# Kernel tuning notes

Measured on AMD Instinct MI355X. Metric: run time of the kernel, lower is better.

Reference implementation:

```python
import jax, jax.numpy as jnp
import numpy as np

NUM_HEADS = 12
EMB = 768
HEAD = 64
SEQ = 2048
BATCH = 2


def setup_inputs() -> dict:
    key = jax.random.key(0)
    ks = jax.random.split(key, 6)
    scale = 0.02
    x = jax.random.normal(ks[0], (BATCH, SEQ, EMB), dtype=jnp.float32)
    # per-head Q/K/V projections (bias-free, Karpathy-style HeadAttention), batched over heads
    Wq = jax.random.normal(ks[1], (NUM_HEADS, EMB, HEAD), dtype=jnp.float32) * scale
    Wk = jax.random.normal(ks[2], (NUM_HEADS, EMB, HEAD), dtype=jnp.float32) * scale
    Wv = jax.random.normal(ks[3], (NUM_HEADS, EMB, HEAD), dtype=jnp.float32) * scale
    # output projection: Linear(head_size*num_heads, emb_size)
    Wo = jax.random.normal(ks[4], (NUM_HEADS * HEAD, EMB), dtype=jnp.float32) * scale
    bo = jax.random.normal(ks[5], (EMB,), dtype=jnp.float32) * scale
    return {"x": x, "Wq": Wq, "Wk": Wk, "Wv": Wv, "Wo": Wo, "bo": bo}


def reference(x, Wq, Wk, Wv, Wo, bo):
    B, S, E = x.shape
    # batched per-head projections: [B,S,E] x [H,E,D] -> [B,H,S,D]
    q = jnp.einsum("bse,hed->bhsd", x, Wq)
    k = jnp.einsum("bse,hed->bhsd", x, Wk)
    v = jnp.einsum("bse,hed->bhsd", x, Wv)
    scale = 1.0 / jnp.sqrt(jnp.asarray(HEAD, dtype=x.dtype))
    scores = jnp.einsum("bhsd,bhtd->bhst", q, k) * scale  # [B,H,S,S]
    causal = jnp.tril(jnp.ones((S, S), dtype=bool))
    scores = jnp.where(causal, scores, jnp.asarray(-jnp.inf, dtype=scores.dtype))
    attn = jax.nn.softmax(scores, axis=-1)
    out = jnp.einsum("bhst,bhtd->bhsd", attn, v)  # [B,H,S,D]
    # concat heads along last dim: [B,S,H*D]
    out = out.transpose(0, 2, 1, 3).reshape(B, S, NUM_HEADS * HEAD)
    # output projection (dropout is identity in eval mode)
    return out @ Wo + bo
```

## Files before the change

kernel.cpp:

```cpp
#include <hip/hip_runtime.h>
#include <hip/hip_bf16.h>
#include <string.h>

#define NHEAD 12
#define EMB 768
#define HDD 64
#define SEQ 2048

typedef __attribute__((ext_vector_type(4))) float f32x4;
typedef __attribute__((ext_vector_type(8))) short short8;
typedef __attribute__((ext_vector_type(4))) short short4v;
typedef __attribute__((ext_vector_type(2))) unsigned uint2v;
typedef unsigned int u32;

#define GLL16(g, l)                                                            \
    __builtin_amdgcn_global_load_lds(                                          \
        (const __attribute__((address_space(1))) u32*)(g),                     \
        (__attribute__((address_space(3))) u32*)(l), 16, 0, 0)

static __device__ __forceinline__ short bf16s(float f) {
    unsigned u = __builtin_bit_cast(unsigned, f);
    u = (u + 0x7fffu + ((u >> 16) & 1u)) >> 16;
    return (short)u;
}
static __device__ __forceinline__ float bf2f(short s) {
    unsigned u = ((unsigned)(unsigned short)s) << 16;
    return __builtin_bit_cast(float, u);
}
static __device__ __forceinline__ float ex2(float x) {
    float r;
    asm("v_exp_f32 %0, %1" : "=v"(r) : "v"(x));
    return r;
}
static __device__ __forceinline__ unsigned pk2(float a, float b) {
    float2 f2;
    f2.x = a;
    f2.y = b;
    __hip_bfloat162 h = __float22bfloat162_rn(f2);
    unsigned r;
    memcpy(&r, &h, 4);
    return r;
}

__global__ void k_cvt_all(const float* __restrict__ x, const float* __restrict__ Wq,
                          const float* __restrict__ Wk, const float* __restrict__ Wv,
                          const float* __restrict__ Wo, short* __restrict__ xb,
                          short* __restrict__ WqT, short* __restrict__ WkT,
                          short* __restrict__ WvT, short* __restrict__ WoT) {
    const int bid = blockIdx.x, t = threadIdx.x;
    if (bid < 1536) {
        const int i = (bid * 256 + t) * 8;
        const f32x4* s = (const f32x4*)(x + i);
        f32x4 a = s[0], b = s[1];
        short8 o;
        o[0] = bf16s(a[0]); o[1] = bf16s(a[1]); o[2] = bf16s(a[2]); o[3] = bf16s(a[3]);
        o[4] = bf16s(b[0]); o[5] = bf16s(b[1]); o[6] = bf16s(b[2]); o[7] = bf16s(b[3]);
        *(short8*)(xb + i) = o;
    } else if (bid < 1968) {
        const int idx = bid - 1536;
        const int h = idx % 12, e0 = ((idx / 12) % 12) * 64, z = idx / 144;
        const float* W = z == 0 ? Wq : (z == 1 ? Wk : Wv);
        short* Wt = z == 0 ? WqT : (z == 1 ? WkT : WvT);
        __shared__ float tile[64][65];
        const int r = t >> 2, c0 = (t & 3) * 16;
        const float* src = W + (h * EMB + e0 + r) * HDD + c0;
#pragma unroll
        for (int i = 0; i < 16; ++i) tile[r][c0 + i] = src[i];
        __syncthreads();
        short* dst = Wt + (h * HDD + r) * EMB + e0 + c0;
#pragma unroll
        for (int i = 0; i < 16; ++i) dst[i] = bf16s(tile[c0 + i][r]);
    } else {
        const int idx = bid - 1968;
        const int k0 = (idx % 12) * 64, n0 = (idx / 12) * 64;
        __shared__ float tile[64][65];
        const int r = t >> 2, c0 = (t & 3) * 16;
        const float* src = Wo + (k0 + r) * EMB + n0 + c0;
#pragma unroll
        for (int i = 0; i < 16; ++i) tile[r][c0 + i] = src[i];
        __syncthreads();
        short* dst = WoT + (n0 + r) * EMB + k0 + c0;
#pragma unroll
        for (int i = 0; i < 16; ++i) dst[i] = bf16s(tile[c0 + i][r]);
    }
}

template <int MODE>
__global__ __launch_bounds__(256) void k_gemm(
        const short* __restrict__ xb, const short* __restrict__ Wt0,
        const short* __restrict__ Wt1, const short* __restrict__ Wt2,
        short* __restrict__ Qo, short* __restrict__ Ko, short* __restrict__ Vo,
        const float* __restrict__ bias, float* __restrict__ Fout) {
    __shared__ alignas(16) short As[2][128 * 32];
    __shared__ alignas(16) short Bs[2][128 * 32];
    const int t = threadIdx.x, lane = t & 63, wave = t >> 6;
    const int z = (MODE == 0) ? blockIdx.z : 0;
    const short* Ap;
    const short* Bp;
    int m0, n0;
    if (MODE == 1) {
        Ap = xb; Bp = Wt0; m0 = blockIdx.y * 128; n0 = blockIdx.x * 128;
    } else if (z == 0) {
        Ap = xb; Bp = Wt0; m0 = blockIdx.y * 128; n0 = blockIdx.x * 128;
    } else if (z == 1) {
        Ap = xb; Bp = Wt1; m0 = blockIdx.y * 128; n0 = blockIdx.x * 128;
    } else {
        Ap = Wt2; Bp = xb; m0 = blockIdx.x * 128; n0 = blockIdx.y * 128;
    }

    const int srow = lane >> 2;
    const int scolSw = ((lane & 3) ^ ((srow >> 1) & 3)) * 8;
    const short* gA = Ap + (long)(m0 + wave * 32 + srow) * EMB + scolSw;
    const short* gB = Bp + (long)(n0 + wave * 32 + srow) * EMB + scolSw;
    const int ldoff = (wave * 32) * 32;

    const int wm = (wave >> 1) * 64, wn = (wave & 1) * 64;
    const int fr = lane & 15, hi = lane >> 4;
    const int rdoff = (hi ^ ((fr >> 1) & 3)) * 8;

    f32x4 acc[4][4];
#pragma unroll
    for (int i = 0; i < 4; ++i)
#pragma unroll
        for (int j = 0; j < 4; ++j)
#pragma unroll
            for (int e = 0; e < 4; ++e) acc[i][j][e] = 0.f;

    GLL16(gA, &As[0][ldoff]);
    GLL16(gA + 16 * EMB, &As[0][ldoff + 16 * 32]);
    GLL16(gB, &Bs[0][ldoff]);
    GLL16(gB + 16 * EMB, &Bs[0][ldoff + 16 * 32]);
    __syncthreads();

    int cur = 0;
    for (int kk = 0; kk < EMB; kk += 32) {
        const int nxt = cur ^ 1;
        if (kk + 32 < EMB) {
            GLL16(gA + kk + 32, &As[nxt][ldoff]);
            GLL16(gA + kk + 32 + 16 * EMB, &As[nxt][ldoff + 16 * 32]);
            GLL16(gB + kk + 32, &Bs[nxt][ldoff]);
            GLL16(gB + kk + 32 + 16 * EMB, &Bs[nxt][ldoff + 16 * 32]);
        }
        const short* curA = &As[cur][0];
        const short* curB = &Bs[cur][0];
        short8 af[4], bfq[4];
#pragma unroll
        for (int i = 0; i < 4; ++i)
            af[i] = *(const short8*)(curA + (wm + i * 16 + fr) * 32 + rdoff);
#pragma unroll
        for (int j = 0; j < 4; ++j)
            bfq[j] = *(const short8*)(curB + (wn + j * 16 + fr) * 32 + rdoff);
#pragma unroll
        for (int i = 0; i < 4; ++i)
#pragma unroll
            for (int j = 0; j < 4; ++j)
                acc[i][j] = __builtin_amdgcn_mfma_f32_16x16x32_bf16(af[i], bfq[j], acc[i][j], 0, 0, 0);
        __syncthreads();
        cur = nxt;
    }

    const int r0 = hi * 4;
#pragma unroll
    for (int i = 0; i < 4; ++i) {
#pragma unroll
        for (int j = 0; j < 4; ++j) {
            const int nbase = n0 + wn + j * 16 + fr;
            float bj = 0.f;
            if (MODE == 1) bj = bias[nbase];
#pragma unroll
            for (int r = 0; r < 4; ++r) {
                const int m = m0 + wm + i * 16 + r0 + r;
                float v = acc[i][j][r];
                if (MODE == 0) {
                    if (z == 2) {
                        const int hh = m >> 6, dd = m & 63;
                        const int bb = nbase >> 11, ss = nbase & 2047;
                        Vo[(long)((bb * NHEAD + hh) * HDD + dd) * SEQ + ss] = bf16s(v);
                    } else {
                        const int bb = m >> 11, ss = m & 2047;
                        const int hh = nbase >> 6, dd = nbase & 63;
                        short* Dst = (z == 0) ? Qo : Ko;
                        if (z == 0) v *= 0.18033688f;
                        Dst[(long)((bb * NHEAD + hh) * SEQ + ss) * HDD + dd] = bf16s(v);
                    }
                } else {
                    Fout[(long)m * EMB + nbase] = v + bj;
                }
            }
        }
    }
}

__global__ __launch_bounds__(256) void k_attn(
        const short* __restrict__ Q, const short* __restrict__ K,
        const short* __restrict__ VT, short* __restrict__ O,
        short* __restrict__ Ub, float* __restrict__ Mb, float* __restrict__ Lb) {
    __shared__ alignas(16) short Kbuf[2][64 * 72];
    __shared__ alignas(16) short Vbuf[2][64 * 72];
    __shared__ alignas(16) short Ps[4][16 * 72];
    const int bh = blockIdx.x;
    const int h = bh % NHEAD, b = bh / NHEAD;
    const int yy = blockIdx.y;
    int qs, kb, ke, chunk, split;
    if (yy < 16)      { qs = 16 + yy; kb = 0;  ke = 16;     chunk = 0; split = 1; }
    else if (yy < 32) { qs = yy;      kb = 16; ke = qs + 1; chunk = 1; split = 1; }
    else              { qs = 47 - yy; kb = 0;  ke = qs + 1; chunk = 0; split = 0; }
    const int q0 = qs * 64;
    const int t = threadIdx.x, lane = t & 63, wave = t >> 6;
    const long base = (long)(b * NHEAD + h) * SEQ * HDD;
    const short* Qg = Q + base;
    const short* Kg = K + base;
    const short* Vg = VT + base;
    const int fr = lane & 15, hi = lane >> 4, fk = hi * 8, r0 = hi * 4;
    const int wq = q0 + wave * 16;

    short8 qf[2];
#pragma unroll
    for (int c = 0; c < 2; ++c)
        qf[c] = *(const short8*)(Qg + (long)(wq + fr) * HDD + c * 32 + fk);

    f32x4 oacc[4];
#pragma unroll
    for (int i = 0; i < 4; ++i)
#pragma unroll
        for (int e = 0; e < 4; ++e) oacc[i][e] = 0.f;
    float mrun = -3e38f, lrun = 0.f;

    const int srow = t >> 2, sc = (t & 3) * 16;
    const short* KgS = Kg + (long)srow * HDD + sc;
    const short* VgS = Vg + (long)srow * SEQ + sc;
    short* Pw = &Ps[wave][0];

    short8 kv0 = *(const short8*)(KgS + (long)(kb * 64) * HDD);
    short8 kv1 = *(const short8*)(KgS + (long)(kb * 64) * HDD + 8);
    short8 vv0 = *(const short8*)(VgS + kb * 64);
    short8 vv1 = *(const short8*)(VgS + kb * 64 + 8);
    *(short8*)(&Kbuf[0][srow * 72 + sc]) = kv0;
    *(short8*)(&Kbuf[0][srow * 72 + sc + 8]) = kv1;
    *(short8*)(&Vbuf[0][srow * 72 + sc]) = vv0;
    *(short8*)(&Vbuf[0][srow * 72 + sc + 8]) = vv1;
    if (ke - kb > 1) {
        kv0 = *(const short8*)(KgS + (long)(kb * 64 + 64) * HDD);
        kv1 = *(const short8*)(KgS + (long)(kb * 64 + 64) * HDD + 8);
        vv0 = *(const short8*)(VgS + kb * 64 + 64);
        vv1 = *(const short8*)(VgS + kb * 64 + 64 + 8);
    }
    __syncthreads();

    for (int kt = kb; kt < ke; ++kt) {
        const int k0 = kt * 64;
        const int cur = (kt - kb) & 1;
        if (kt + 1 < ke) {
            *(short8*)(&Kbuf[cur ^ 1][srow * 72 + sc]) = kv0;
            *(short8*)(&Kbuf[cur ^ 1][srow * 72 + sc + 8]) = kv1;
            *(short8*)(&Vbuf[cur ^ 1][srow * 72 + sc]) = vv0;
            *(short8*)(&Vbuf[cur ^ 1][srow * 72 + sc + 8]) = vv1;
            if (kt + 2 < ke) {
                kv0 = *(const short8*)(KgS + (long)(k0 + 128) * HDD);
                kv1 = *(const short8*)(KgS + (long)(k0 + 128) * HDD + 8);
                vv0 = *(const short8*)(VgS + (k0 + 128));
                vv1 = *(const short8*)(VgS + (k0 + 128) + 8);
            }
        }
        if (k0 <= wq + 15) {
            const short* Ks = &Kbuf[cur][0];
            const short* Vs = &Vbuf[cur][0];

            f32x4 st[4];
#pragma unroll
            for (int nt = 0; nt < 4; ++nt) {
                const short8 kf0 = *(const short8*)(Ks + (nt * 16 + fr) * 72 + fk);
                const short8 kf1 = *(const short8*)(Ks + (nt * 16 + fr) * 72 + 32 + fk);
#pragma unroll
                for (int e = 0; e < 4; ++e) st[nt][e] = 0.f;
                st[nt] = __builtin_amdgcn_mfma_f32_16x16x32_bf16(kf0, qf[0], st[nt], 0, 0, 0);
                st[nt] = __builtin_amdgcn_mfma_f32_16x16x32_bf16(kf1, qf[1], st[nt], 0, 0, 0);
            }

            float p[4][4];
            float pmax = -3e38f;
            if (k0 + 63 > wq) {
                const int myq = wq + fr;
#pragma unroll
                for (int nt = 0; nt < 4; ++nt)
#pragma unroll
                    for (int r = 0; r < 4; ++r) {
                        float s = st[nt][r];
                        if (k0 + nt * 16 + r0 + r > myq) s = -3e38f;
                        p[nt][r] = s;
                        pmax = fmaxf(pmax, s);
                    }
            } else {
#pragma unroll
                for (int nt = 0; nt < 4; ++nt)
#pragma unroll
                    for (int r = 0; r < 4; ++r) {
                        p[nt][r] = st[nt][r];
                        pmax = fmaxf(pmax, st[nt][r]);
                    }
            }
            pmax = fmaxf(pmax, __shfl_xor(pmax, 16, 64));
            pmax = fmaxf(pmax, __shfl_xor(pmax, 32, 64));
            const float mnew = fmaxf(mrun, pmax);
            const float corr = ex2(mrun - mnew);
            mrun = mnew;
            float rsum = 0.f;
#pragma unroll
            for (int nt = 0; nt < 4; ++nt)
#pragma unroll
                for (int r = 0; r < 4; ++r) {
                    const float e = ex2(p[nt][r] - mnew);
                    p[nt][r] = e;
                    rsum += e;
                }
            rsum += __shfl_xor(rsum, 16, 64);
            rsum += __shfl_xor(rsum, 32, 64);
            lrun = lrun * corr + rsum;
#pragma unroll
            for (int dt = 0; dt < 4; ++dt)
#pragma unroll
                for (int e = 0; e < 4; ++e) oacc[dt][e] *= corr;

#pragma unroll
            for (int nt = 0; nt < 4; ++nt) {
                uint2v w;
                w[0] = pk2(p[nt][0], p[nt][1]);
                w[1] = pk2(p[nt][2], p[nt][3]);
                *(uint2v*)(Pw + fr * 72 + nt * 16 + r0) = w;
            }

#pragma unroll
            for (int kc = 0; kc < 2; ++kc) {
                const short8 pf = *(const short8*)(Pw + fr * 72 + kc * 32 + fk);
#pragma unroll
                for (int dt = 0; dt < 4; ++dt) {
                    const short8 vf = *(const short8*)(Vs + (dt * 16 + fr) * 72 + kc * 32 + fk);
                    oacc[dt] = __builtin_amdgcn_mfma_f32_16x16x32_bf16(vf, pf, oacc[dt], 0, 0, 0);
                }
            }
        }
        __syncthreads();
    }

    if (split) {
        const int pidx = (bh * 16 + (qs - 16)) * 2 + chunk;
        short* Up = Ub + pidx * 4096;
#pragma unroll
        for (int dt = 0; dt < 4; ++dt)
#pragma unroll
            for (int r = 0; r < 4; ++r)
                Up[(dt * 16 + r0 + r) * 64 + wave * 16 + fr] = bf16s(oacc[dt][r]);
        if (lane < 16) {
            Mb[pidx * 64 + wave * 16 + lane] = mrun;
            Lb[pidx * 64 + wave * 16 + lane] = lrun;
        }
        return;
    }

    short* Os = &Ps[0][0];
    const float iv = 1.0f / lrun;
#pragma unroll
    for (int dt = 0; dt < 4; ++dt) {
        uint2v w;
        w[0] = pk2(oacc[dt][0] * iv, oacc[dt][1] * iv);
        w[1] = pk2(oacc[dt][2] * iv, oacc[dt][3] * iv);
        *(uint2v*)(Os + (wave * 16 + fr) * 72 + dt * 16 + r0) = w;
    }
    __syncthreads();
    {
        const int row = t >> 2, c0 = (t & 3) * 16;
        const short8 o0 = *(const short8*)(Os + row * 72 + c0);
        const short8 o1 = *(const short8*)(Os + row * 72 + c0 + 8);
        short* Og = O + (long)(b * SEQ + q0 + row) * EMB + h * HDD + c0;
        *(short8*)Og = o0;
        *(short8*)(Og + 8) = o1;
    }
}

__global__ __launch_bounds__(256) void k_merge(
        const short* __restrict__ Ub, const float* __restrict__ Mb,
        const float* __restrict__ Lb, short* __restrict__ O) {
    __shared__ float aS[64], bS[64], iL[64];
    __shared__ short tile[64 * 72];
    const int bid = blockIdx.x;
    const int bh = bid >> 4, sidx = bid & 15;
    const int h = bh % NHEAD, b = bh / NHEAD;
    const int q0 = (16 + sidx) * 64;
    const int p0 = (bh * 16 + sidx) * 2, p1 = p0 + 1;
    const int t = threadIdx.x;
    if (t < 64) {
        const float m1 = Mb[p0 * 64 + t], m2 = Mb[p1 * 64 + t];
        const float l1 = Lb[p0 * 64 + t], l2 = Lb[p1 * 64 + t];
        const float m = fmaxf(m1, m2);
        const float a = ex2(m1 - m), bb = ex2(m2 - m);
        aS[t] = a;
        bS[t] = bb;
        iL[t] = 1.0f / (l1 * a + l2 * bb);
    }
    __syncthreads();
    {
        const int d = t >> 2, qg = (t & 3) * 16;
        const short8 u1a = *(const short8*)(Ub + p0 * 4096 + d * 64 + qg);
        const short8 u1b = *(const short8*)(Ub + p0 * 4096 + d * 64 + qg + 8);
        const short8 u2a = *(const short8*)(Ub + p1 * 4096 + d * 64 + qg);
        const short8 u2b = *(const short8*)(Ub + p1 * 4096 + d * 64 + qg + 8);
#pragma unroll
        for (int i = 0; i < 8; ++i) {
            const int q = qg + i;
            tile[q * 72 + d] = bf16s((bf2f(u1a[i]) * aS[q] + bf2f(u2a[i]) * bS[q]) * iL[q]);
        }
#pragma unroll
        for (int i = 0; i < 8; ++i) {
            const int q = qg + 8 + i;
            tile[q * 72 + d] = bf16s((bf2f(u1b[i]) * aS[q] + bf2f(u2b[i]) * bS[q]) * iL[q]);
        }
    }
    __syncthreads();
    {
        const int q = t >> 2, dg = (t & 3) * 16;
        const short8 o0 = *(const short8*)(tile + q * 72 + dg);
        const short8 o1 = *(const short8*)(tile + q * 72 + dg + 8);
        short* Og = O + (long)(b * SEQ + q0 + q) * EMB + h * HDD + dg;
        *(short8*)Og = o0;
        *(short8*)(Og + 8) = o1;
    }
}

extern "C" void kernel_launch(void* const* d_in, const int* in_sizes, int n_in,
                              void* d_out, int out_size, void* d_ws, size_t ws_size,
                              hipStream_t stream) {
    const float* x  = (const float*)d_in[0];
    const float* Wq = (const float*)d_in[1];
    const float* Wk = (const float*)d_in[2];
    const float* Wv = (const float*)d_in[3];
    const float* Wo = (const float*)d_in[4];
    const float* bo = (const float*)d_in[5];
    float* out = (float*)d_out;

    char* ws = (char*)d_ws;
    short* xb  = (short*)(ws + 0);
    short* WqT = (short*)(ws + 6291456);
    short* WkT = (short*)(ws + 7471104);
    short* WvT = (short*)(ws + 8650752);
    short* WoT = (short*)(ws + 9830400);
    short* Qb  = (short*)(ws + 11010048);
    short* Kb  = (short*)(ws + 17301504);
    short* VTb = (short*)(ws + 23592960);
    short* Ob  = (short*)(ws + 29884416);
    short* Ub  = (short*)(ws + 0);
    float* Mb  = (float*)(ws + 6291456);
    float* Lb  = (float*)(ws + 6488064);

    k_cvt_all<<<dim3(2112), dim3(256), 0, stream>>>(
        x, Wq, Wk, Wv, Wo, xb, WqT, WkT, WvT, WoT);
    k_gemm<0><<<dim3(6, 32, 3), dim3(256), 0, stream>>>(
        xb, WqT, WkT, WvT, Qb, Kb, VTb, (const float*)nullptr, (float*)nullptr);
    k_attn<<<dim3(24, 48), dim3(256), 0, stream>>>(Qb, Kb, VTb, Ob, Ub, Mb, Lb);
    k_merge<<<dim3(384), dim3(256), 0, stream>>>(Ub, Mb, Lb, Ob);
    k_gemm<1><<<dim3(6, 32, 1), dim3(256), 0, stream>>>(
        Ob, WoT, (const short*)nullptr, (const short*)nullptr,
        (short*)nullptr, (short*)nullptr, (short*)nullptr, bo, out);
}
```

Measured before the change: 95.53 us.

## Double attention query tile to 128 rows per block, reusing K/V fragments

Each attention block now processes 128 query rows, with every wave owning 32 rows as two 16-row sub-tiles. K fragments are loaded once from LDS per tile and reused for both sub-tiles, and V fragments feed two MFMA chains. This halves per-row staging of K/V through LDS. The causal split scheme and merge kernel are resized to 128-row strips, halving the grid. The trade-off is higher register pressure and fewer blocks (576 vs 1152), which reduces parallelism and load balance.

```diff
diff --git a/kernel.cpp b/kernel.cpp
--- a/kernel.cpp
+++ b/kernel.cpp
@@ -201,30 +201,34 @@
     const int bh = blockIdx.x;
     const int h = bh % NHEAD, b = bh / NHEAD;
     const int yy = blockIdx.y;
-    int qs, kb, ke, chunk, split;
-    if (yy < 16)      { qs = 16 + yy; kb = 0;  ke = 16;     chunk = 0; split = 1; }
-    else if (yy < 32) { qs = yy;      kb = 16; ke = qs + 1; chunk = 1; split = 1; }
-    else              { qs = 47 - yy; kb = 0;  ke = qs + 1; chunk = 0; split = 0; }
-    const int q0 = qs * 64;
+    int strip, kb, ke, chunk, split;
+    if (yy < 8)       { strip = 8 + yy;  kb = 0;  ke = 16;          chunk = 0; split = 1; }
+    else if (yy < 16) { strip = 23 - yy; kb = 16; ke = 2 * strip + 2; chunk = 1; split = 1; }
+    else              { strip = 23 - yy; kb = 0;  ke = 2 * strip + 2; chunk = 0; split = 0; }
+    const int q0 = strip * 128;
     const int t = threadIdx.x, lane = t & 63, wave = t >> 6;
     const long base = (long)(b * NHEAD + h) * SEQ * HDD;
     const short* Qg = Q + base;
     const short* Kg = K + base;
     const short* Vg = VT + base;
     const int fr = lane & 15, hi = lane >> 4, fk = hi * 8, r0 = hi * 4;
-    const int wq = q0 + wave * 16;
-
-    short8 qf[2];
-#pragma unroll
-    for (int c = 0; c < 2; ++c)
-        qf[c] = *(const short8*)(Qg + (long)(wq + fr) * HDD + c * 32 + fk);
-
-    f32x4 oacc[4];
-#pragma unroll
-    for (int i = 0; i < 4; ++i)
-#pragma unroll
-        for (int e = 0; e < 4; ++e) oacc[i][e] = 0.f;
-    float mrun = -3e38f, lrun = 0.f;
+    const int wq = q0 + wave * 32;
+
+    short8 qf[2][2];
+#pragma unroll
+    for (int qi = 0; qi < 2; ++qi)
+#pragma unroll
+        for (int c = 0; c < 2; ++c)
+            qf[qi][c] = *(const short8*)(Qg + (long)(wq + qi * 16 + fr) * HDD + c * 32 + fk);
+
+    f32x4 oacc[2][4];
+#pragma unroll
+    for (int qi = 0; qi < 2; ++qi)
+#pragma unroll
+        for (int i = 0; i < 4; ++i)
+#pragma unroll
+            for (int e = 0; e < 4; ++e) oacc[qi][i][e] = 0.f;
+    float mrun[2] = {-3e38f, -3e38f}, lrun[2] = {0.f, 0.f};
 
     const int srow = t >> 2, sc = (t & 3) * 16;
     const short* KgS = Kg + (long)srow * HDD + sc;
@@ -262,80 +266,92 @@
                 vv1 = *(const short8*)(VgS + (k0 + 128) + 8);
             }
         }
-        if (k0 <= wq + 15) {
+        if (k0 <= wq + 31) {
             const short* Ks = &Kbuf[cur][0];
             const short* Vs = &Vbuf[cur][0];
 
-            f32x4 st[4];
+            short8 kf[4][2];
 #pragma unroll
             for (int nt = 0; nt < 4; ++nt) {
-                const short8 kf0 = *(const short8*)(Ks + (nt * 16 + fr) * 72 + fk);
-                const short8 kf1 = *(const short8*)(Ks + (nt * 16 + fr) * 72 + 32 + fk);
-#pragma unroll
-                for (int e = 0; e < 4; ++e) st[nt][e] = 0.f;
-                st[nt] = __builtin_amdgcn_mfma_f32_16x16x32_bf16(kf0, qf[0], st[nt], 0, 0, 0);
-                st[nt] = __builtin_amdgcn_mfma_f32_16x16x32_bf16(kf1, qf[1], st[nt], 0, 0, 0);
-            }
-
-            float p[4][4];
-            float pmax = -3e38f;
-            if (k0 + 63 > wq) {
-                const int myq = wq + fr;
+                kf[nt][0] = *(const short8*)(Ks + (nt * 16 + fr) * 72 + fk);
+                kf[nt][1] = *(const short8*)(Ks + (nt * 16 + fr) * 72 + 32 + fk);
+            }
+
+            short8 pfq[2][2];
+#pragma unroll
+            for (int qi = 0; qi < 2; ++qi) {
+                const int qbase = wq + qi * 16;
+                f32x4 st[4];
+#pragma unroll
+                for (int nt = 0; nt < 4; ++nt) {
+#pragma unroll
+                    for (int e = 0; e < 4; ++e) st[nt][e] = 0.f;
+                    st[nt] = __builtin_amdgcn_mfma_f32_16x16x32_bf16(kf[nt][0], qf[qi][0], st[nt], 0, 0, 0);
+                    st[nt] = __builtin_amdgcn_mfma_f32_16x16x32_bf16(kf[nt][1], qf[qi][1], st[nt], 0, 0, 0);
+                }
+
+                float p[4][4];
+                float pmax = -3e38f;
+                if (k0 + 63 > qbase) {
+                    const int myq = qbase + fr;
+#pragma unroll
+                    for (int nt = 0; nt < 4; ++nt)
+#pragma unroll
+                        for (int r = 0; r < 4; ++r) {
+                            float s = st[nt][r];
+                            if (k0 + nt * 16 + r0 + r > myq) s = -3e38f;
+                            p[nt][r] = s;
+                            pmax = fmaxf(pmax, s);
+                        }
+                } else {
+#pragma unroll
+                    for (int nt = 0; nt < 4; ++nt)
+#pragma unroll
+                        for (int r = 0; r < 4; ++r) {
+                            p[nt][r] = st[nt][r];
+                            pmax = fmaxf(pmax, st[nt][r]);
+                        }
+                }
+                pmax = fmaxf(pmax, __shfl_xor(pmax, 16, 64));
+                pmax = fmaxf(pmax, __shfl_xor(pmax, 32, 64));
+                const float mnew = fmaxf(mrun[qi], pmax);
+                const float corr = ex2(mrun[qi] - mnew);
+                mrun[qi] = mnew;
+                float rsum = 0.f;
 #pragma unroll
                 for (int nt = 0; nt < 4; ++nt)
 #pragma unroll
                     for (int r = 0; r < 4; ++r) {
-                        float s = st[nt][r];
-                        if (k0 + nt * 16 + r0 + r > myq) s = -3e38f;
-                        p[nt][r] = s;
-                        pmax = fmaxf(pmax, s);
+                        const float e = ex2(p[nt][r] - mnew);
+                        p[nt][r] = e;
+                        rsum += e;
                     }
-            } else {
-#pragma unroll
-                for (int nt = 0; nt < 4; ++nt)
-#pragma unroll
-                    for (int r = 0; r < 4; ++r) {
-                        p[nt][r] = st[nt][r];
-                        pmax = fmaxf(pmax, st[nt][r]);
-                    }
-            }
-            pmax = fmaxf(pmax, __shfl_xor(pmax, 16, 64));
-            pmax = fmaxf(pmax, __shfl_xor(pmax, 32, 64));
-            const float mnew = fmaxf(mrun, pmax);
-            const float corr = ex2(mrun - mnew);
-            mrun = mnew;
-            float rsum = 0.f;
-#pragma unroll
-            for (int nt = 0; nt < 4; ++nt)
-#pragma unroll
-                for (int r = 0; r < 4; ++r) {
-                    const float e = ex2(p[nt][r] - mnew);
-                    p[nt][r] = e;
-                    rsum += e;
+                rsum += __shfl_xor(rsum, 16, 64);
+                rsum += __shfl_xor(rsum, 32, 64);
+                lrun[qi] = lrun[qi] * corr + rsum;
+#pragma unroll
+                for (int dt = 0; dt < 4; ++dt)
+#pragma unroll
+                    for (int e = 0; e < 4; ++e) oacc[qi][dt][e] *= corr;
+
+#pragma unroll
+                for (int nt = 0; nt < 4; ++nt) {
+                    uint2v w;
+                    w[0] = pk2(p[nt][0], p[nt][1]);
+                    w[1] = pk2(p[nt][2], p[nt][3]);
+                    *(uint2v*)(Pw + fr * 72 + nt * 16 + r0) = w;
                 }
-            rsum += __shfl_xor(rsum, 16, 64);
-            rsum += __shfl_xor(rsum, 32, 64);
-            lrun = lrun * corr + rsum;
-#pragma unroll
-            for (int dt = 0; dt < 4; ++dt)
-#pragma unroll
-                for (int e = 0; e < 4; ++e) oacc[dt][e] *= corr;
-
-#pragma unroll
-            for (int nt = 0; nt < 4; ++nt) {
-                uint2v w;
-                w[0] = pk2(p[nt][0], p[nt][1]);
-                w[1] = pk2(p[nt][2], p[nt][3]);
-                *(uint2v*)(Pw + fr * 72 + nt * 16 + r0) = w;
+                pfq[qi][0] = *(const short8*)(Pw + fr * 72 + fk);
+                pfq[qi][1] = *(const short8*)(Pw + fr * 72 + 32 + fk);
             }
 
 #pragma unroll
             for (int kc = 0; kc < 2; ++kc) {
-                const short8 pf = *(const short8*)(Pw + fr * 72 + kc * 32 + fk);
 #pragma unroll
                 for (int dt = 0; dt < 4; ++dt) {
                     const short8 vf = *(const short8*)(Vs + (dt * 16 + fr) * 72 + kc * 32 + fk);
-                    oacc[dt] = __builtin_amdgcn_mfma_f32_16x16x32_bf16(vf, pf, oacc[dt], 0, 0, 0);
+                    oacc[0][dt] = __builtin_amdgcn_mfma_f32_16x16x32_bf16(vf, pfq[0][kc], oacc[0][dt], 0, 0, 0);
+                    oacc[1][dt] = __builtin_amdgcn_mfma_f32_16x16x32_bf16(vf, pfq[1][kc], oacc[1][dt], 0, 0, 0);
                 }
             }
         }
@@ -343,54 +359,66 @@
     }
 
     if (split) {
-        const int pidx = (bh * 16 + (qs - 16)) * 2 + chunk;
-        short* Up = Ub + pidx * 4096;
-#pragma unroll
-        for (int dt = 0; dt < 4; ++dt)
-#pragma unroll
-            for (int r = 0; r < 4; ++r)
-                Up[(dt * 16 + r0 + r) * 64 + wave * 16 + fr] = bf16s(oacc[dt][r]);
+        const int pidx = (bh * 8 + (strip - 8)) * 2 + chunk;
+        short* Up = Ub + pidx * 8192;
+#pragma unroll
+        for (int qi = 0; qi < 2; ++qi)
+#pragma unroll
+            for (int dt = 0; dt < 4; ++dt)
+#pragma unroll
+                for (int r = 0; r < 4; ++r)
+                    Up[(dt * 16 + r0 + r) * 128 + wave * 32 + qi * 16 + fr] = bf16s(oacc[qi][dt][r]);
         if (lane < 16) {
-            Mb[pidx * 64 + wave * 16 + lane] = mrun;
-            Lb[pidx * 64 + wave * 16 + lane] = lrun;
+#pragma unroll
+            for (int qi = 0; qi < 2; ++qi) {
+                Mb[pidx * 128 + wave * 32 + qi * 16 + lane] = mrun[qi];
+                Lb[pidx * 128 + wave * 32 + qi * 16 + lane] = lrun[qi];
+            }
         }
         return;
     }
 
-    short* Os = &Ps[0][0];
-    const float iv = 1.0f / lrun;
-#pragma unroll
-    for (int dt = 0; dt < 4; ++dt) {
-        uint2v w;
-        w[0] = pk2(oacc[dt][0] * iv, oacc[dt][1] * iv);
-        w[1] = pk2(oacc[dt][2] * iv, oacc[dt][3] * iv);
-        *(uint2v*)(Os + (wave * 16 + fr) * 72 + dt * 16 + r0) = w;
+    short* Os = &Kbuf[0][0];
+#pragma unroll
+    for (int qi = 0; qi < 2; ++qi) {
+        const float iv = 1.0f / lrun[qi];
+#pragma unroll
+        for (int dt = 0; dt < 4; ++dt) {
+            uint2v w;
+            w[0] = pk2(oacc[qi][dt][0] * iv, oacc[qi][dt][1] * iv);
+            w[1] = pk2(oacc[qi][dt][2] * iv, oacc[qi][dt][3] * iv);
+            *(uint2v*)(Os + (wave * 32 + qi * 16 + fr) * 72 + dt * 16 + r0) = w;
+        }
     }
     __syncthreads();
     {
-        const int row = t >> 2, c0 = (t & 3) * 16;
-        const short8 o0 = *(const short8*)(Os + row * 72 + c0);
-        const short8 o1 = *(const short8*)(Os + row * 72 + c0 + 8);
-        short* Og = O + (long)(b * SEQ + q0 + row) * EMB + h * HDD + c0;
+        const int row = t >> 1, half = t & 1;
+        const short8 o0 = *(const short8*)(Os + row * 72 + half * 32);
+        const short8 o1 = *(const short8*)(Os + row * 72 + half * 32 + 8);
+        const short8 o2 = *(const short8*)(Os + row * 72 + half * 32 + 16);
+        const short8 o3 = *(const short8*)(Os + row * 72 + half * 32 + 24);
+        short* Og = O + (long)(b * SEQ + q0 + row) * EMB + h * HDD + half * 32;
         *(short8*)Og = o0;
         *(short8*)(Og + 8) = o1;
+        *(short8*)(Og + 16) = o2;
+        *(short8*)(Og + 24) = o3;
     }
 }
 
 __global__ __launch_bounds__(256) void k_merge(
         const short* __restrict__ Ub, const float* __restrict__ Mb,
         const float* __restrict__ Lb, short* __restrict__ O) {
-    __shared__ float aS[64], bS[64], iL[64];
-    __shared__ short tile[64 * 72];
+    __shared__ float aS[128], bS[128], iL[128];
+    __shared__ short tile[128 * 72];
     const int bid = blockIdx.x;
-    const int bh = bid >> 4, sidx = bid & 15;
+    const int bh = bid >> 3, sidx = bid & 7;
     const int h = bh % NHEAD, b = bh / NHEAD;
-    const int q0 = (16 + sidx) * 64;
-    const int p0 = (bh * 16 + sidx) * 2, p1 = p0 + 1;
+    const int q0 = (8 + sidx) * 128;
+    const int p0 = (bh * 8 + sidx) * 2, p1 = p0 + 1;
     const int t = threadIdx.x;
-    if (t < 64) {
-        const float m1 = Mb[p0 * 64 + t], m2 = Mb[p1 * 64 + t];
-        const float l1 = Lb[p0 * 64 + t], l2 = Lb[p1 * 64 + t];
+    if (t < 128) {
+        const float m1 = Mb[p0 * 128 + t], m2 = Mb[p1 * 128 + t];
+        const float l1 = Lb[p0 * 128 + t], l2 = Lb[p1 * 128 + t];
         const float m = fmaxf(m1, m2);
         const float a = ex2(m1 - m), bb = ex2(m2 - m);
         aS[t] = a;
@@ -399,30 +427,30 @@
     }
     __syncthreads();
     {
-        const int d = t >> 2, qg = (t & 3) * 16;
-        const short8 u1a = *(const short8*)(Ub + p0 * 4096 + d * 64 + qg);
-        const short8 u1b = *(const short8*)(Ub + p0 * 4096 + d * 64 + qg + 8);
-        const short8 u2a = *(const short8*)(Ub + p1 * 4096 + d * 64 + qg);
-        const short8 u2b = *(const short8*)(Ub + p1 * 4096 + d * 64 + qg + 8);
-#pragma unroll
-        for (int i = 0; i < 8; ++i) {
-            const int q = qg + i;
-            tile[q * 72 + d] = bf16s((bf2f(u1a[i]) * aS[q] + bf2f(u2a[i]) * bS[q]) * iL[q]);
-        }
-#pragma unroll
-        for (int i = 0; i < 8; ++i) {
-            const int q = qg + 8 + i;
-            tile[q * 72 + d] = bf16s((bf2f(u1b[i]) * aS[q] + bf2f(u2b[i]) * bS[q]) * iL[q]);
+        const int d = t >> 2, qg = (t & 3) * 32;
+#pragma unroll
+        for (int j = 0; j < 4; ++j) {
+            const short8 u1 = *(const short8*)(Ub + p0 * 8192 + d * 128 + qg + j * 8);
+            const short8 u2 = *(const short8*)(Ub + p1 * 8192 + d * 128 + qg + j * 8);
+#pragma unroll
+            for (int i = 0; i < 8; ++i) {
+                const int q = qg + j * 8 + i;
+                tile[q * 72 + d] = bf16s((bf2f(u1[i]) * aS[q] + bf2f(u2[i]) * bS[q]) * iL[q]);
+            }
         }
     }
     __syncthreads();
     {
-        const int q = t >> 2, dg = (t & 3) * 16;
-        const short8 o0 = *(const short8*)(tile + q * 72 + dg);
-        const short8 o1 = *(const short8*)(tile + q * 72 + dg + 8);
-        short* Og = O + (long)(b * SEQ + q0 + q) * EMB + h * HDD + dg;
+        const int row = t >> 1, half = t & 1;
+        const short8 o0 = *(const short8*)(tile + row * 72 + half * 32);
+        const short8 o1 = *(const short8*)(tile + row * 72 + half * 32 + 8);
+        const short8 o2 = *(const short8*)(tile + row * 72 + half * 32 + 16);
+        const short8 o3 = *(const short8*)(tile + row * 72 + half * 32 + 24);
+        short* Og = O + (long)(b * SEQ + q0 + row) * EMB + h * HDD + half * 32;
         *(short8*)Og = o0;
         *(short8*)(Og + 8) = o1;
+        *(short8*)(Og + 16) = o2;
+        *(short8*)(Og + 24) = o3;
     }
 }
 
@@ -455,8 +483,8 @@
         x, Wq, Wk, Wv, Wo, xb, WqT, WkT, WvT, WoT);
     k_gemm<0><<<dim3(6, 32, 3), dim3(256), 0, stream>>>(
         xb, WqT, WkT, WvT, Qb, Kb, VTb, (const float*)nullptr, (float*)nullptr);
-    k_attn<<<dim3(24, 48), dim3(256), 0, stream>>>(Qb, Kb, VTb, Ob, Ub, Mb, Lb);
-    k_merge<<<dim3(384), dim3(256), 0, stream>>>(Ub, Mb, Lb, Ob);
+    k_attn<<<dim3(24, 24), dim3(256), 0, stream>>>(Qb, Kb, VTb, Ob, Ub, Mb, Lb);
+    k_merge<<<dim3(192), dim3(256), 0, stream>>>(Ub, Mb, Lb, Ob);
     k_gemm<1><<<dim3(6, 32, 1), dim3(256), 0, stream>>>(
         Ob, WoT, (const short*)nullptr, (const short*)nullptr,
         (short*)nullptr, (short*)nullptr, (short*)nullptr, bo, out);
```

Result: slower. 101.1 us (+5.8%).
